# Kernel optimization log

Hardware: AMD Instinct MI355X
Metric: run time of the kernel (lower is better)

Reference implementation:

```python
import jax, jax.numpy as jnp
from jax import lax
import numpy as np

B, A, T = 128, 32, 32
HID = 64
DEG = 7
MODES = 25
OUT_FRAMES = 12
NHEAD, DHEAD = 16, 64


def legendre_tmat(out_frames, degree):
    # normalized Legendre basis evaluated at t_n, shape [degree+1, len(t_n)]
    t = np.arange(-6, out_frames + 1, dtype=np.float32)
    t = t / t[-1]
    P = [np.ones_like(t), t]
    for n in range(1, degree):
        P.append(((2 * n + 1) * t * P[n] - n * P[n - 1]) / (n + 1))
    P = np.stack(P[: degree + 1], 0)
    norm = np.sqrt((2 * np.arange(degree + 1) + 1) / 2.0).astype(np.float32)
    return (P * norm[:, None]).astype(np.float32)


def _conv(x, w, stride, pad):
    return lax.conv_general_dilated(x, w, (stride, stride), [(pad, pad), (pad, pad)],
                                    dimension_numbers=("NCHW", "OIHW", "NCHW"))


def _bn(x, g, b, eps=1e-5):
    m = jnp.mean(x, axis=(0, 2, 3), keepdims=True)
    v = jnp.var(x, axis=(0, 2, 3), keepdims=True)
    return (x - m) / jnp.sqrt(v + eps) * g[None, :, None, None] + b[None, :, None, None]


def setup_inputs() -> dict:
    key = jax.random.key(0)
    ks = jax.random.split(key, 32)

    def rn(i, shape, scale=0.05):
        return jax.random.normal(ks[i], shape, dtype=jnp.float32) * scale

    inp = {
        "cnn_feat": rn(0, (B, 1024, 14, 14), 1.0),
        "ego_state": rn(1, (B, T, 5), 1.0),
        "agents_state": rn(2, (B, A, T, 5), 1.0),
        "ego_state_len": jax.random.randint(ks[3], (B,), 0, T),
        "agents_state_len": jax.random.randint(ks[4], (B, A), 0, T),
        "agents_grid_pos": jax.random.randint(ks[5], (B, A, 2), 0, 14),
        "state_fc_W": rn(6, (HID, 5)), "state_fc_b": rn(7, (HID,)),
        "lstm_Wih": rn(8, (4 * HID, HID)), "lstm_Whh": rn(9, (4 * HID, HID)),
        "lstm_bih": rn(10, (4 * HID,)), "lstm_bhh": rn(11, (4 * HID,)),
        "enc_fc_W": rn(12, (HID, HID)), "enc_fc_b": rn(13, (HID,)),
        "conv1_W": rn(14, (512, 1024 + HID, 3, 3)),
        "bn1_g": jnp.ones((512,), jnp.float32), "bn1_b": jnp.zeros((512,), jnp.float32),
        "conv2_W": rn(15, (512, 512, 3, 3)),
        "bn2_g": jnp.ones((512,), jnp.float32), "bn2_b": jnp.zeros((512,), jnp.float32),
        "q_W": rn(16, (NHEAD * DHEAD, 512 + HID)),
        "k_W": rn(17, (NHEAD * DHEAD, 512, 1, 1)),
        "v_W": rn(18, (NHEAD * DHEAD, 512, 1, 1)),
        "attn_out_W": rn(19, (512, NHEAD * DHEAD)), "attn_out_b": rn(20, (512,)),
        "cls_W": rn(21, (MODES, 512 + HID + 512)), "cls_b": rn(22, (MODES,)),
        "dec1_W": rn(23, (256, 512 + HID + 512)), "dec1_b": rn(24, (256,)),
        "dec2_W": rn(25, ((DEG + 1) * 2 * MODES, 256)), "dec2_b": rn(26, ((DEG + 1) * 2 * MODES,)),
    }
    return inp


def reference(cnn_feat, ego_state, agents_state, ego_state_len, agents_state_len,
              agents_grid_pos, state_fc_W, state_fc_b, lstm_Wih, lstm_Whh, lstm_bih,
              lstm_bhh, enc_fc_W, enc_fc_b, conv1_W, bn1_g, bn1_b, conv2_W, bn2_g,
              bn2_b, q_W, k_W, v_W, attn_out_W, attn_out_b, cls_W, cls_b, dec1_W,
              dec1_b, dec2_W, dec2_b):
    Bn, _, Hs, Ws = cnn_feat.shape

    def lstm_encode(seq, lens):
        # seq [N,T,5]; packed-sequence semantics with zero init == take h at step len-1
        N, Tn, _ = seq.shape
        h = seq @ state_fc_W.T + state_fc_b  # [N,T,64]

        def step(carry, xt):
            hh, cc = carry
            g = xt @ lstm_Wih.T + hh @ lstm_Whh.T + lstm_bih + lstm_bhh
            i, f_, gg, o = jnp.split(g, 4, axis=-1)
            cc = jax.nn.sigmoid(f_) * cc + jax.nn.sigmoid(i) * jnp.tanh(gg)
            hh = jax.nn.sigmoid(o) * jnp.tanh(cc)
            return (hh, cc), hh

        z = jnp.zeros((N, HID), h.dtype)
        _, hs = lax.scan(step, (z, z), h.transpose(1, 0, 2))  # hs [T,N,64]
        idx = jnp.clip(lens, 1, Tn).astype(jnp.int32) - 1
        last = hs[idx, jnp.arange(N)]
        return last @ enc_fc_W.T + enc_fc_b

    ego = lstm_encode(ego_state, ego_state_len)  # [B,64]
    ag = lstm_encode(agents_state.reshape(Bn * A, T, 5),
                     agents_state_len.reshape(-1)).reshape(Bn, A, HID)

    # scatter-add agent encodings into the spatial grid (overlapping writes accumulate)
    grid = jnp.zeros((Bn, Hs, Ws, HID), cnn_feat.dtype)
    bidx = jnp.broadcast_to(jnp.arange(Bn)[:, None], (Bn, A))
    grid = grid.at[bidx, agents_grid_pos[..., 0], agents_grid_pos[..., 1]].add(ag)

    x = jnp.concatenate([cnn_feat, grid.transpose(0, 3, 1, 2)], axis=1)
    x = jax.nn.relu(_bn(_conv(x, conv1_W, 1, 1), bn1_g, bn1_b))
    x = jax.nn.relu(_bn(_conv(x, conv2_W, 2, 1), bn2_g, bn2_b))  # [B,512,7,7]

    ego_t = jnp.concatenate([x[:, :, 3, 3], ego], axis=1)  # [B,576]
    q = (ego_t @ q_W.T).reshape(Bn, NHEAD, DHEAD)
    k = _conv(x, k_W, 1, 1).reshape(Bn, NHEAD, DHEAD, -1)  # g = 9*9 = 81
    v = _conv(x, v_W, 1, 1).reshape(Bn, NHEAD, DHEAD, -1)
    energy = jnp.einsum("bhf,bhfg->bhg", q, k)
    attn = jax.nn.softmax(energy / (NHEAD * DHEAD) ** 0.5, axis=2)
    o = jnp.einsum("bhg,bhdg->bhd", attn, v).reshape(Bn, -1)
    o = o @ attn_out_W.T + attn_out_b

    feat = jnp.concatenate([o, ego_t], axis=1)  # [B,1088]
    conf = feat @ cls_W.T + cls_b
    d = jax.nn.relu(feat @ dec1_W.T + dec1_b)
    d = (d @ dec2_W.T + dec2_b).reshape(Bn, MODES, -1)

    tmat = jnp.asarray(legendre_tmat(OUT_FRAMES, DEG))  # [DEG+1, 19]
    out_x = d[:, :, : DEG + 1] @ tmat
    out_y = d[:, :, DEG + 1:] @ tmat
    traj = jnp.stack([out_x, out_y], axis=3)  # [B,MODES,19,2]
    return traj, conf
```

## Files before the change

kernel.cpp:

```cpp
#include <hip/hip_runtime.h>
#include <stdint.h>
#include <stddef.h>

#define DEVINL static __device__ __forceinline__

typedef __attribute__((ext_vector_type(8))) short  bfrag;
typedef __attribute__((ext_vector_type(4))) float  facc;

DEVINL uint16_t f2b(float f){
  uint32_t u = __float_as_uint(f);
  return (uint16_t)((u + 0x7fffu + ((u >> 16) & 1u)) >> 16);
}
DEVINL float b2f(uint16_t b){ return __uint_as_float(((uint32_t)b) << 16); }

DEVINL facc MFMA(bfrag a, bfrag b, facc c){
  return __builtin_amdgcn_mfma_f32_16x16x32_bf16(a, b, c, 0, 0, 0);
}

DEVINL void gload16(const void* g, void* l){
  __builtin_amdgcn_global_load_lds(
      (const __attribute__((address_space(1))) uint32_t*)g,
      (__attribute__((address_space(3))) uint32_t*)l, 16, 0, 0);
}

DEVINL float fast_tanh(float x){
  return 2.f/(1.f+__expf(-2.f*x)) - 1.f;
}

struct PrepArgs {
  const float* cnn;        uint16_t* Xp;
  uint16_t* Y1P;           float* gridb;   float* stats;
  const float *Wih, *Whh, *bih, *bhh, *sW, *sb, *encW;
  uint16_t* Wc;  float* be;  uint16_t* encWb;  float* tm;
  const float* conv1W;     uint16_t* WP1;
  const float* conv2W;     uint16_t* WP2;
  const float* kWf;        uint16_t* WKT;
  const float* fs[6];      uint16_t* fd[6];   int fn[6];  int fb0[6];
};

__global__ __launch_bounds__(256) void k_prep(PrepArgs a){
  int blk = blockIdx.x, t = threadIdx.x;
  if(blk < 4096){
    __shared__ float tile[32*200];
    int b = blk>>5, ch = blk&31;
    int c0 = ch*32;
    for(int i=t;i<32*196;i+=256){
      int ci = i/196, s = i%196;
      tile[ci*200+s] = a.cnn[((size_t)b*1024 + c0+ci)*196 + s];
    }
    __syncthreads();
    for(int i=t;i<16*196;i+=256){
      int s = i>>4, c2 = i&15;
      int y = s/14, x = s%14;
      uint32_t pu = (uint32_t)f2b(tile[(2*c2)*200+s]) |
                    ((uint32_t)f2b(tile[(2*c2+1)*200+s])<<16);
      *(uint32_t*)(a.Xp + (((size_t)b*16 + y+1)*16 + x+1)*1088 + c0 + 2*c2) = pu;
    }
  } else if(blk < 4352){
    int idx = blk - 4096;
    int b = idx & 127;
    uint16_t* base = (idx < 128) ? a.Xp : a.Y1P;
    int C = (idx < 128) ? 1088 : 512;
    for(int p=0;p<60;p++){
      int y, x;
      if(p<16){ y=0; x=p; }
      else if(p<32){ y=15; x=p-16; }
      else { int q=p-32; y=1+(q>>1); x=(q&1)?15:0; }
      uint32_t* dst = (uint32_t*)(base + ((size_t)(b*16+y)*16 + x)*C);
      for(int i=t;i<C/2;i+=256) dst[i] = 0;
    }
    float* g = a.gridb + (size_t)idx*6272;
    for(int i=t;i<6272;i+=256) g[i] = 0.f;
    if(idx == 0){
      for(int i=t;i<2048;i+=256) a.stats[i] = 0.f;
    }
  } else if(blk == 4352){
    int n = t;
    if(n < 19){
      float tv = (float)(n - 6) / 12.0f;
      float Pm = 1.0f, Pc = tv;
      a.tm[0*19+n] = Pm * sqrtf(0.5f);
      a.tm[1*19+n] = Pc * sqrtf(1.5f);
      for(int q=1; q<7; q++){
        float Pn = ((float)(2*q+1)*tv*Pc - (float)q*Pm) / (float)(q+1);
        Pm = Pc; Pc = Pn;
        a.tm[(q+1)*19+n] = Pc * sqrtf((float)(2*(q+1)+1) * 0.5f);
      }
    }
    for(int k=0;k<64;k++) a.Wc[n*96+k] = f2b(a.Whh[n*64+k]);
    for(int k5=0;k5<5;k5++){
      float s = 0.f;
      for(int j=0;j<64;j++) s += a.Wih[n*64+j]*a.sW[j*5+k5];
      a.Wc[n*96+64+k5] = f2b(s);
    }
    for(int k=69;k<96;k++) a.Wc[n*96+k] = 0;
    float s = 0.f;
    for(int j=0;j<64;j++) s += a.Wih[n*64+j]*a.sb[j];
    a.be[n] = s + a.bih[n] + a.bhh[n];
    if(n < 64){
      for(int k=0;k<64;k++) a.encWb[n*64+k] = f2b(a.encW[n*64+k]);
    }
  } else if(blk < 4865){
    int o = blk - 4353;
    for(int c=t; c<1088; c+=256){
      const float* src = a.conv1W + ((size_t)o*1088 + c)*9;
      float v[9];
      #pragma unroll
      for(int d=0;d<9;d++) v[d] = src[d];
      #pragma unroll
      for(int d=0;d<9;d++)
        a.WP1[((size_t)d*512 + o)*1088 + c] = f2b(v[d]);
    }
  } else if(blk < 5377){
    int o = blk - 4865;
    for(int c=t; c<512; c+=256){
      const float* src = a.conv2W + ((size_t)o*512 + c)*9;
      float v[9];
      #pragma unroll
      for(int d=0;d<9;d++) v[d] = src[d];
      #pragma unroll
      for(int dy=0;dy<3;dy++)
        #pragma unroll
        for(int dx=0;dx<3;dx++)
          a.WP2[((size_t)(dy*512 + o))*1536 + dx*512 + c] = f2b(v[dy*3+dx]);
    }
  } else if(blk < 5393){
    int h = blk - 5377;
    for(int i=t; i<32768; i+=256){
      int c = i>>6, d = i&63;
      a.WKT[((size_t)h*512 + c)*64 + d] = f2b(a.kWf[((size_t)(h*64+d))*512 + c]);
    }
  } else {
    int fblk = blk - 5393;
    int j = 0;
    while(j < 5 && fblk >= a.fb0[j+1]) j++;
    int base = (fblk - a.fb0[j])*8192;
    const float* s = a.fs[j];
    uint16_t* d = a.fd[j];
    int n = a.fn[j];
    int hi = base + 8192; if(hi > n) hi = n;
    for(int i=base+t; i<hi; i+=256) d[i] = f2b(s[i]);
  }
}

__global__ void k_packx_grid(const float* __restrict__ agrid, uint16_t* __restrict__ Xp)
{
  int b = blockIdx.x >> 1, half = blockIdx.x & 1;
  int j0 = half*32, t = threadIdx.x;
  for(int i=t;i<16*196;i+=256){
    int s = i>>4, j2 = i&15;
    int y = s/14, x = s%14;
    const float* gsrc = agrid + ((size_t)b*196 + s)*64 + j0 + 2*j2;
    uint32_t pu = (uint32_t)f2b(gsrc[0]) | ((uint32_t)f2b(gsrc[1])<<16);
    *(uint32_t*)(Xp + (((size_t)b*16 + y+1)*16 + x+1)*1088 + 1024 + j0 + 2*j2) = pu;
  }
}

__global__ __launch_bounds__(256) void k_lstm(
    const float* __restrict__ ego_seq, const float* __restrict__ ag_seq,
    const int* __restrict__ ego_len, const int* __restrict__ ag_len,
    const int* __restrict__ grid_pos,
    const uint16_t* __restrict__ Wc, const float* __restrict__ be,
    const uint16_t* __restrict__ encWb, const float* __restrict__ encB,
    float* __restrict__ agrid, uint16_t* __restrict__ egoT, uint16_t* __restrict__ feat)
{
  __shared__ __align__(16) uint16_t A[32*96];
  __shared__ float Xf[32*160];
  __shared__ int   idxs[32];

  int t = threadIdx.x, w = t>>6, l = t&63;
  int blk = blockIdx.x;
  bool isEgo = blk < 4;
  int seq0 = isEgo ? blk*32 : (blk-4)*32;
  const float* seqp = (isEgo ? ego_seq : ag_seq) + (size_t)seq0*160;

  for(int i=t;i<32*160;i+=256) Xf[i] = seqp[i];
  if(t < 32){
    int L = isEgo ? ego_len[seq0+t] : ag_len[seq0+t];
    if(L < 1) L = 1;
    idxs[t] = L-1;
  }
  for(int i=t;i<32*96;i+=256) A[i] = 0;

  bfrag bf[4][3];
  float be4[4];
  for(int ct=0;ct<4;ct++){
    int n = (ct*4+w)*16 + (l&15);
    for(int ks=0;ks<3;ks++)
      bf[ct][ks] = *(const bfrag*)(Wc + n*96 + ks*32 + (l>>4)*8);
    be4[ct] = be[n];
  }
  float cst[8], hl[8];
  for(int i=0;i<8;i++){ cst[i]=0.f; hl[i]=0.f; }
  __syncthreads();
  int myidx[8];
  for(int rt=0;rt<2;rt++) for(int r=0;r<4;r++){
    int s = rt*16 + (l>>4)*4 + r;
    myidx[rt*4+r] = idxs[s];
  }

  for(int st=0; st<32; st++){
    if(t < 160){ int s=t/5, kk=t%5; A[s*96+64+kk] = f2b(Xf[s*160 + st*5 + kk]); }
    __syncthreads();
    facc acc[2][4];
    for(int rt=0;rt<2;rt++) for(int ct=0;ct<4;ct++) acc[rt][ct] = facc{0.f,0.f,0.f,0.f};
    #pragma unroll
    for(int ks=0;ks<3;ks++){
      bfrag aA[2];
      #pragma unroll
      for(int rt=0;rt<2;rt++)
        aA[rt] = *(const bfrag*)(A + (rt*16+(l&15))*96 + ks*32 + (l>>4)*8);
      #pragma unroll
      for(int rt=0;rt<2;rt++)
        #pragma unroll
        for(int ct=0;ct<4;ct++)
          acc[rt][ct] = MFMA(aA[rt], bf[ct][ks], acc[rt][ct]);
    }
    __syncthreads();
    #pragma unroll
    for(int rt=0;rt<2;rt++) for(int r=0;r<4;r++){
      int cell = rt*4+r;
      int s = rt*16 + (l>>4)*4 + r;
      float gi = acc[rt][0][r] + be4[0];
      float gf = acc[rt][1][r] + be4[1];
      float gg = acc[rt][2][r] + be4[2];
      float go = acc[rt][3][r] + be4[3];
      float si = 1.f/(1.f+__expf(-gi));
      float sf = 1.f/(1.f+__expf(-gf));
      float so = 1.f/(1.f+__expf(-go));
      float tg = fast_tanh(gg);
      float c2 = sf*cst[cell] + si*tg;
      cst[cell] = c2;
      float hn = so*fast_tanh(c2);
      A[s*96 + w*16 + (l&15)] = f2b(hn);
      if(st == myidx[cell]) hl[cell] = hn;
    }
  }
  __syncthreads();
  for(int rt=0;rt<2;rt++) for(int r=0;r<4;r++){
    int s = rt*16 + (l>>4)*4 + r;
    A[s*96 + w*16 + (l&15)] = f2b(hl[rt*4+r]);
  }
  __syncthreads();
  bfrag eb[2];
  for(int ks=0;ks<2;ks++)
    eb[ks] = *(const bfrag*)(encWb + (w*16+(l&15))*64 + ks*32 + (l>>4)*8);
  facc ea[2]; ea[0] = facc{0.f,0.f,0.f,0.f}; ea[1] = facc{0.f,0.f,0.f,0.f};
  for(int ks=0;ks<2;ks++){
    for(int rt=0;rt<2;rt++){
      bfrag aA = *(const bfrag*)(A + (rt*16+(l&15))*96 + ks*32 + (l>>4)*8);
      ea[rt] = MFMA(aA, eb[ks], ea[rt]);
    }
  }
  int n = w*16 + (l&15);
  float bn_ = encB[n];
  for(int rt=0;rt<2;rt++) for(int r=0;r<4;r++){
    int s = rt*16 + (l>>4)*4 + r;
    float v = ea[rt][r] + bn_;
    int gs = seq0 + s;
    if(isEgo){
      egoT[(size_t)gs*576 + 512 + n] = f2b(v);
      feat[(size_t)gs*1088 + 1024 + n] = f2b(v);
    } else {
      int py = grid_pos[gs*2+0], px = grid_pos[gs*2+1];
      atomicAdd(&agrid[((size_t)(gs>>5)*196 + py*14 + px)*64 + n], v);
    }
  }
}

__global__ __launch_bounds__(512) void k_conv1_8p(
    const uint16_t* __restrict__ Ain, const uint16_t* __restrict__ Wb,
    uint16_t* __restrict__ Out, float* __restrict__ stats)
{
  constexpr int CB = 1088;
  constexpr int NSTEP = 153;
  __shared__ __align__(16) char LDSb[131072];

  int t = threadIdx.x, w = t>>6, l = t&63;
  int wm = w>>2, wn = w&3;

  int xcd = blockIdx.x & 7, pos = blockIdx.x >> 3;
  int wgid = (xcd < 4 ? xcd*25 : 100 + (xcd-4)*24) + pos;
  int m0 = (wgid % 98) * 256;
  int n0 = (wgid / 98) * 256;

  const uint16_t* aP[2][2];
  const uint16_t* bP[2][2];
  #pragma unroll
  for(int P=0;P<2;P++)
    #pragma unroll
    for(int j=0;j<2;j++){
      int partrow = j*64 + (t>>3);
      int swz = ((t&7) ^ (partrow&7))*8;
      int gr = P*64 + partrow + ((partrow>=64)?64:0);
      int m = m0 + gr; int b = m/196, s = m%196, y = s/14, x = s%14;
      aP[P][j] = Ain + ((b*16+y)*16+x)*CB + swz;
      int nb = n0 + (partrow>>5)*64 + P*32 + (partrow&31);
      bP[P][j] = Wb + (size_t)nb*CB + swz;
    }

  facc acc[8][4];
  #pragma unroll
  for(int i=0;i<8;i++)
    #pragma unroll
    for(int j=0;j<4;j++) acc[i][j] = facc{0.f,0.f,0.f,0.f};

  bfrag aF[4][2], bF0[2][2], bF1[2][2];
  int dd = 0;

  #define STG(buf, PART) do{                                                   \
    if((PART)==0 || (PART)==3){ const int P_ = ((PART)==3);                    \
      _Pragma("unroll")                                                        \
      for(int j_=0;j_<2;j_++)                                                  \
        gload16(aP[P_][j_], LDSb + (buf)*65536 + P_*16384 + j_*8192 + w*1024); \
    } else { const int P_ = ((PART)==2);                                       \
      _Pragma("unroll")                                                        \
      for(int j_=0;j_<2;j_++)                                                  \
        gload16(bP[P_][j_], LDSb + (buf)*65536 + 32768 + P_*16384 + j_*8192 + w*1024); \
    }                                                                          \
  }while(0)

  #define ADVK() do{                                                          \
    if(dd==8){                                                                \
      _Pragma("unroll")                                                       \
      for(int P_=0;P_<2;P_++) for(int j_=0;j_<2;j_++){                        \
        aP[P_][j_] += 64 - 34*CB; bP[P_][j_] += 64 - 8*512*CB; }              \
      dd = 0;                                                                 \
    } else {                                                                  \
      int sA_ = (dd==2||dd==5) ? 14*CB : CB;                                  \
      _Pragma("unroll")                                                       \
      for(int P_=0;P_<2;P_++) for(int j_=0;j_<2;j_++){                        \
        aP[P_][j_] += sA_; bP[P_][j_] += 512*CB; }                            \
      dd++;                                                                   \
    }                                                                         \
  }while(0)

  #define VM4 asm volatile("s_waitcnt vmcnt(4)" ::: "memory")
  #define VM2 asm volatile("s_waitcnt vmcnt(2)" ::: "memory")
  #define VM0 asm volatile("s_waitcnt vmcnt(0)" ::: "memory")

  #define LDA(mh) do{                                                         \
    const uint16_t* Ab_ = (const uint16_t*)(LDSb + p*65536 + (mh)*16384);     \
    _Pragma("unroll")                                                         \
    for(int i_=0;i_<4;i_++)                                                   \
      _Pragma("unroll")                                                       \
      for(int ks_=0;ks_<2;ks_++)                                              \
        aF[i_][ks_] = *(const bfrag*)(Ab_ + (wm*64 + i_*16 + (l&15))*64       \
                        + ((ks_*32 + (l>>4)*8) ^ ((l&7)<<3)));                \
  }while(0)

  #define LDB(dst, nh) do{                                                   \
    const uint16_t* Bb_ = (const uint16_t*)(LDSb + p*65536 + 32768 + (nh)*16384); \
    _Pragma("unroll")                                                         \
    for(int j_=0;j_<2;j_++)                                                   \
      _Pragma("unroll")                                                       \
      for(int ks_=0;ks_<2;ks_++)                                              \
        dst[j_][ks_] = *(const bfrag*)(Bb_ + (wn*32 + j_*16 + (l&15))*64      \
                        + ((ks_*32 + (l>>4)*8) ^ ((l&7)<<3)));                \
  }while(0)

  #define MM(mh, nh, bsrc) do{                                               \
    __builtin_amdgcn_s_setprio(1);                                           \
    _Pragma("unroll")                                                        \
    for(int ks_=0;ks_<2;ks_++)                                               \
      _Pragma("unroll")                                                      \
      for(int i_=0;i_<4;i_++)                                                \
        _Pragma("unroll")                                                    \
        for(int j_=0;j_<2;j_++)                                              \
          acc[(mh)*4+i_][(nh)*2+j_] =                                        \
            MFMA(aF[i_][ks_], bsrc[j_][ks_], acc[(mh)*4+i_][(nh)*2+j_]);     \
    __builtin_amdgcn_s_setprio(0);                                           \
  }while(0)

  #define BARS do{ __builtin_amdgcn_sched_barrier(0); __builtin_amdgcn_s_barrier(); }while(0)
  #define EBAR __builtin_amdgcn_s_barrier()

  STG(0,0); STG(0,1); STG(0,2); STG(0,3);
  ADVK();
  VM4;
  EBAR;

  for(int kt=0; kt<NSTEP-1; kt++){
    int p = kt&1;
    LDA(0); LDB(bF0,0); STG(p^1,0); BARS; MM(0,0,bF0); VM4; EBAR;
    LDB(bF1,1);         STG(p^1,1); BARS; MM(0,1,bF1); VM4; EBAR;
    LDA(1);             STG(p^1,2); BARS; MM(1,1,bF1);      EBAR;
                        STG(p^1,3); BARS; MM(1,0,bF0); VM4; EBAR;
    if(kt < NSTEP-2) ADVK();
  }
  {
    int p = 0;
    LDA(0); LDB(bF0,0); BARS; MM(0,0,bF0); VM2; EBAR;
    LDB(bF1,1);         BARS; MM(0,1,bF1); VM0; EBAR;
    LDA(1);             BARS; MM(1,1,bF1);      EBAR;
                        BARS; MM(1,0,bF0);      EBAR;
  }

  #undef LDA
  #undef LDB
  #undef MM
  #undef BARS
  #undef EBAR
  #undef STG
  #undef ADVK

  __syncthreads();
  int* oo = (int*)LDSb;
  if(t < 256){
    int m = m0 + t; int b = m/196, s = m%196, y = s/14, x = s%14;
    oo[t] = ((b*16 + y+1)*16 + (x+1))*512;
  }
  __syncthreads();
  #pragma unroll
  for(int i=0;i<8;i++)
    #pragma unroll
    for(int j=0;j<4;j++){
      int n = n0 + wn*64 + j*16 + (l&15);
      #pragma unroll
      for(int r=0;r<4;r++){
        int mr = wm*128 + i*16 + (l>>4)*4 + r;
        Out[(size_t)oo[mr] + n] = f2b(acc[i][j][r]);
      }
    }
  __syncthreads();
  float* sred = (float*)LDSb;
  int rg = wm*4 + (l>>4);
  #pragma unroll
  for(int j=0;j<4;j++){
    float s=0.f, q=0.f;
    #pragma unroll
    for(int i=0;i<8;i++)
      #pragma unroll
      for(int r=0;r<4;r++){ float v = acc[i][j][r]; s += v; q += v*v; }
    int nl = wn*64 + j*16 + (l&15);
    sred[(nl*8 + rg)*2+0] = s;
    sred[(nl*8 + rg)*2+1] = q;
  }
  __syncthreads();
  if(t < 256){
    float s=0.f, q=0.f;
    #pragma unroll
    for(int rgi=0;rgi<8;rgi++){ s += sred[(t*8+rgi)*2]; q += sred[(t*8+rgi)*2+1]; }
    atomicAdd(&stats[n0+t], s);
    atomicAdd(&stats[512+n0+t], q);
  }
}

__global__ __launch_bounds__(256) void k_conv2dy(
    const uint16_t* __restrict__ Ain, const uint16_t* __restrict__ Wb,
    uint16_t* __restrict__ PS,
    const float* __restrict__ stats, const float* __restrict__ gg,
    const float* __restrict__ bb)
{
  __shared__ __align__(16) uint16_t As[2*128*64];
  __shared__ __align__(16) uint16_t Bs[2*128*64];
  __shared__ float scs[512], shs[512];

  int t = threadIdx.x, w = t>>6, l = t&63;
  int dy = blockIdx.y;

  for(int c=t;c<512;c+=256){
    float mu = stats[c]*(1.f/25088.f);
    float var = stats[512+c]*(1.f/25088.f) - mu*mu;
    float sc = gg[c]*rsqrtf(var+1e-5f);
    scs[c] = sc; shs[c] = bb[c] - mu*sc;
  }

  int xcd = blockIdx.x & 7, pos = blockIdx.x >> 3;
  int wgid = (xcd < 4 ? xcd*25 : 100 + (xcd-4)*24) + pos;
  int n0 = (wgid / 49) * 128;
  int m0 = (wgid % 49) * 128;

  const uint16_t* aP[4];
  const uint16_t* bP[4];
  #pragma unroll
  for(int p=0;p<4;p++){
    int r = w*32 + p*8 + (l>>3);
    int m = m0 + r;
    int b = m/49, s = m%49, y = s/7, x = s%7;
    aP[p] = Ain + ((b*16 + 2*y + dy)*16 + 2*x)*512 + (l&7)*8;
    bP[p] = Wb + ((size_t)(dy*512 + n0 + r))*1536 + (l&7)*8;
  }

  facc acc[4][4];
  #pragma unroll
  for(int i=0;i<4;i++)
    #pragma unroll
    for(int j=0;j<4;j++) acc[i][j] = facc{0.f,0.f,0.f,0.f};
  int wm = w>>1, wn = w&1;

  uint4 av[4];

  #define C2LOADA() do{                                                     \
    _Pragma("unroll")                                                       \
    for(int p=0;p<4;p++){ av[p] = *(const uint4*)aP[p]; aP[p] += 64; }      \
  }while(0)

  #define C2BSTG(buf) do{                                                  \
    char* bd_ = (char*)Bs + (buf)*16384 + w*4096;                          \
    _Pragma("unroll")                                                      \
    for(int p=0;p<4;p++){ gload16(bP[p], bd_ + p*1024); bP[p] += 64; }     \
  }while(0)

  #define C2AWRITE(buf, kt) do{                                            \
    int c0_ = (((kt)*64) & 511) + (l&7)*8;                                  \
    _Pragma("unroll")                                                      \
    for(int p=0;p<4;p++){                                                  \
      const uint16_t* vv = (const uint16_t*)&av[p];                        \
      uint16_t ov[8];                                                      \
      _Pragma("unroll")                                                    \
      for(int j=0;j<8;j++){                                                \
        int c_ = c0_ + j;                                                  \
        ov[j] = f2b(fmaxf(b2f(vv[j])*scs[c_] + shs[c_], 0.f));             \
      }                                                                    \
      *(uint4*)((char*)As + (buf)*16384 + w*4096 + p*1024 + l*16) = *(uint4*)ov; \
    }                                                                      \
  }while(0)

  #define C2CMP(buf) do{                                                    \
    const uint16_t* Ab_ = As + (buf)*8192;                                  \
    const uint16_t* Bb_ = Bs + (buf)*8192;                                  \
    _Pragma("unroll")                                                       \
    for(int ks=0;ks<2;ks++){                                                \
      bfrag a_[4], b_[4];                                                   \
      _Pragma("unroll")                                                     \
      for(int i=0;i<4;i++)                                                  \
        a_[i] = *(const bfrag*)(Ab_ + (wm*64 + i*16 + (l&15))*64 + ks*32 + (l>>4)*8); \
      _Pragma("unroll")                                                     \
      for(int j=0;j<4;j++)                                                  \
        b_[j] = *(const bfrag*)(Bb_ + (wn*64 + j*16 + (l&15))*64 + ks*32 + (l>>4)*8); \
      _Pragma("unroll")                                                     \
      for(int i=0;i<4;i++)                                                  \
        _Pragma("unroll")                                                   \
        for(int j=0;j<4;j++)                                                \
          acc[i][j] = MFMA(a_[i], b_[j], acc[i][j]);                        \
    }                                                                       \
  }while(0)

  C2LOADA();
  C2BSTG(0);
  C2AWRITE(0, 0);
  __syncthreads();
  for(int stp=0; stp<24; stp++){
    if(stp < 23){ C2LOADA(); C2BSTG((stp+1)&1); }
    C2CMP(stp&1);
    if(stp < 23) C2AWRITE((stp+1)&1, stp+1);
    __syncthreads();
  }

  #undef C2LOADA
  #undef C2BSTG
  #undef C2AWRITE
  #undef C2CMP

  uint16_t* out = PS + (size_t)dy*3211264;
  #pragma unroll
  for(int i=0;i<4;i++)
    #pragma unroll
    for(int j=0;j<4;j++){
      int n = n0 + wn*64 + j*16 + (l&15);
      #pragma unroll
      for(int r=0;r<4;r++){
        int mr = m0 + wm*64 + i*16 + (l>>4)*4 + r;
        out[(size_t)mr*512 + n] = f2b(acc[i][j][r]);
      }
    }
}

__global__ void k_bn2sum(const uint16_t* __restrict__ PS, uint16_t* __restrict__ Y2,
                         float* __restrict__ stats)
{
  int t = threadIdx.x;
  int m0 = blockIdx.x*16;
  float s0=0,s1=0,q0=0,q1=0;
  for(int i=0;i<16;i++){
    size_t off = (size_t)(m0+i)*512 + 2*t;
    uint32_t u0 = *(const uint32_t*)(PS + off);
    uint32_t u1 = *(const uint32_t*)(PS + 3211264 + off);
    uint32_t u2 = *(const uint32_t*)(PS + 6422528 + off);
    float a = b2f((uint16_t)u0)+b2f((uint16_t)u1)+b2f((uint16_t)u2);
    float c = b2f((uint16_t)(u0>>16))+b2f((uint16_t)(u1>>16))+b2f((uint16_t)(u2>>16));
    s0+=a; q0+=a*a; s1+=c; q1+=c*c;
    *(uint32_t*)(Y2 + off) = (uint32_t)f2b(a) | ((uint32_t)f2b(c)<<16);
  }
  atomicAdd(&stats[2*t],   s0);
  atomicAdd(&stats[2*t+1], s1);
  atomicAdd(&stats[512+2*t],   q0);
  atomicAdd(&stats[512+2*t+1], q1);
}

__global__ void k_center(const uint16_t* __restrict__ Y2, const float* __restrict__ stats,
                         const float* __restrict__ gg, const float* __restrict__ bb,
                         uint16_t* __restrict__ egoT, uint16_t* __restrict__ feat)
{
  int b = blockIdx.x, t = threadIdx.x;
  int c = 2*t;
  float mu0 = stats[c]*(1.f/6272.f),     mu1 = stats[c+1]*(1.f/6272.f);
  float v0 = stats[512+c]*(1.f/6272.f) - mu0*mu0;
  float v1 = stats[512+c+1]*(1.f/6272.f) - mu1*mu1;
  float sc0 = gg[c]*rsqrtf(v0+1e-5f),    sc1 = gg[c+1]*rsqrtf(v1+1e-5f);
  float sh0 = bb[c] - mu0*sc0,           sh1 = bb[c+1] - mu1*sc1;
  size_t off = (size_t)(b*49+24)*512 + c;
  uint32_t u = *(const uint32_t*)(Y2 + off);
  float a = fmaxf(b2f((uint16_t)u)*sc0 + sh0, 0.f);
  float d = fmaxf(b2f((uint16_t)(u>>16))*sc1 + sh1, 0.f);
  uint32_t pu = (uint32_t)f2b(a) | ((uint32_t)f2b(d)<<16);
  *(uint32_t*)(egoT + (size_t)b*576 + c) = pu;
  *(uint32_t*)(feat + (size_t)b*1088 + 512 + c) = pu;
}

__global__ __launch_bounds__(256) void k_sgemm(
    const uint16_t* __restrict__ A, int lda,
    const uint16_t* __restrict__ B, int ldb,
    const float* __restrict__ bias,
    void* __restrict__ C, int ldc,
    int N, int K, int flags)
{
  int t = threadIdx.x, w = t>>6, l = t&63;
  int nt = blockIdx.x*4 + w;
  int n  = nt*16 + (l&15);
  int m0 = blockIdx.y*16;
  bool nv = n < N;
  facc acc = facc{0.f,0.f,0.f,0.f};
  for(int k=0;k<K;k+=32){
    bfrag af = *(const bfrag*)(A + (size_t)(m0+(l&15))*lda + k + (l>>4)*8);
    bfrag bf_ = {0,0,0,0,0,0,0,0};
    if(nv) bf_ = *(const bfrag*)(B + (size_t)n*ldb + k + (l>>4)*8);
    acc = MFMA(af, bf_, acc);
  }
  if(nv){
    float bv = bias ? bias[n] : 0.f;
    #pragma unroll
    for(int r=0;r<4;r++){
      int m = m0 + (l>>4)*4 + r;
      float v = acc[r] + bv;
      if(flags & 1) v = fmaxf(v, 0.f);
      if(flags & 2) ((float*)C)[(size_t)m*ldc + n] = v;
      else ((uint16_t*)C)[(size_t)m*ldc + n] = f2b(v);
    }
  }
}

__global__ __launch_bounds__(256) void k_tail1(
    const uint16_t* __restrict__ FEAT,
    const uint16_t* __restrict__ D1W, const float* __restrict__ d1B,
    const uint16_t* __restrict__ CLSW, const float* __restrict__ clsB,
    uint16_t* __restrict__ D1out, float* __restrict__ confOut)
{
  int t = threadIdx.x, w = t>>6, l = t&63;
  int m0 = blockIdx.y*16;
  bool isCls = (blockIdx.x == 4);
  int n = (isCls ? w : (blockIdx.x*4 + w))*16 + (l&15);
  int N = isCls ? 25 : 256;
  const uint16_t* B = isCls ? CLSW : D1W;
  bool nv = n < N;
  facc acc = facc{0.f,0.f,0.f,0.f};
  for(int k=0;k<1088;k+=32){
    bfrag af = *(const bfrag*)(FEAT + (size_t)(m0+(l&15))*1088 + k + (l>>4)*8);
    bfrag bf_ = {0,0,0,0,0,0,0,0};
    if(nv) bf_ = *(const bfrag*)(B + (size_t)n*1088 + k + (l>>4)*8);
    acc = MFMA(af, bf_, acc);
  }
  if(nv){
    #pragma unroll
    for(int r=0;r<4;r++){
      int m = m0 + (l>>4)*4 + r;
      if(isCls){
        confOut[(size_t)m*25 + n] = acc[r] + clsB[n];
      } else {
        D1out[(size_t)m*256 + n] = f2b(fmaxf(acc[r] + d1B[n], 0.f));
      }
    }
  }
}

__global__ __launch_bounds__(256) void k_tail2(
    const uint16_t* __restrict__ D1B, const uint16_t* __restrict__ D2W,
    const float* __restrict__ d2B, const float* __restrict__ tm,
    float* __restrict__ outF)
{
  __shared__ float co[16*64];
  __shared__ float tms[152];
  int t = threadIdx.x, w = t>>6, l = t&63;
  if(t < 152) tms[t] = tm[t];
  int bx = blockIdx.x, m0 = blockIdx.y*16;
  int n = (bx*4 + w)*16 + (l&15);
  bool nv = n < 400;
  facc acc = facc{0.f,0.f,0.f,0.f};
  for(int k=0;k<256;k+=32){
    bfrag af = *(const bfrag*)(D1B + (size_t)(m0+(l&15))*256 + k + (l>>4)*8);
    bfrag bf_ = {0,0,0,0,0,0,0,0};
    if(nv) bf_ = *(const bfrag*)(D2W + (size_t)n*256 + k + (l>>4)*8);
    acc = MFMA(af, bf_, acc);
  }
  if(nv){
    #pragma unroll
    for(int r=0;r<4;r++){
      int mm = (l>>4)*4 + r;
      co[mm*64 + (w*16 + (l&15))] = acc[r] + d2B[n];
    }
  }
  __syncthreads();
  int nmodes = (bx < 6) ? 4 : 1;
  for(int idx=t; idx<16*nmodes*19; idx+=256){
    int mm = idx/(nmodes*19);
    int rem = idx%(nmodes*19);
    int md = rem/19, tt = rem%19;
    const float* cp = &co[mm*64 + md*16];
    float x=0.f, y=0.f;
    #pragma unroll
    for(int j=0;j<8;j++){ float tv = tms[j*19+tt]; x += cp[j]*tv; y += cp[8+j]*tv; }
    float* op = outF + ((size_t)(m0+mm)*25 + bx*4+md)*38;
    op[tt*2+0] = x; op[tt*2+1] = y;
  }
}

__global__ __launch_bounds__(256) void k_bgemm(
    const uint16_t* __restrict__ A, int lda, int aoffs,
    const uint16_t* __restrict__ B, int ldb, int brows,
    uint16_t* __restrict__ C, int ldc, int coffs,
    int K)
{
  int t = threadIdx.x, w = t>>6, l = t&63;
  int z = blockIdx.z;
  int n = (blockIdx.x*4 + w)*16 + (l&15);
  int m0 = blockIdx.y*16;
  const uint16_t* Ab = A + (size_t)z*aoffs;
  const uint16_t* Bb = B + (size_t)z*brows*ldb;
  facc acc = facc{0.f,0.f,0.f,0.f};
  for(int k=0;k<K;k+=32){
    bfrag af = *(const bfrag*)(Ab + (size_t)(m0+(l&15))*lda + k + (l>>4)*8);
    bfrag bf_ = *(const bfrag*)(Bb + (size_t)n*ldb + k + (l>>4)*8);
    acc = MFMA(af, bf_, acc);
  }
  #pragma unroll
  for(int r=0;r<4;r++){
    int m = m0 + (l>>4)*4 + r;
    C[(size_t)m*ldc + z*coffs + n] = f2b(acc[r]);
  }
}

__global__ __launch_bounds__(512) void k_attn2(
    const uint16_t* __restrict__ U16, const uint16_t* __restrict__ y2,
    const float* __restrict__ stats, const float* __restrict__ gg,
    const float* __restrict__ bb,
    uint16_t* __restrict__ zout)
{
  __shared__ __align__(16) char LA[49*1024 + 8*1024];
  __shared__ float scs[512], shs[512];
  uint16_t* uls = (uint16_t*)(LA + 49*1024);
  int t = threadIdx.x, w = t>>6, l = t&63;
  int b = blockIdx.x >> 1, half = blockIdx.x & 1;
  int h = half*8 + w;

  if(t < 512){
    float mu = stats[t]*(1.f/6272.f);
    float var = stats[512+t]*(1.f/6272.f) - mu*mu;
    float sc = gg[t]*rsqrtf(var+1e-5f);
    scs[t] = sc; shs[t] = bb[t] - mu*sc;
  }
  __syncthreads();

  for(int i=t; i<3136; i+=512){
    int g = i>>6, c16 = i&63;
    uint4 raw = *(const uint4*)(y2 + ((size_t)(b*49+g)*512 + c16*8));
    const uint16_t* rp = (const uint16_t*)&raw;
    uint16_t ov[8];
    #pragma unroll
    for(int j=0;j<8;j++){
      int c = c16*8 + j;
      ov[j] = f2b(fmaxf(b2f(rp[j])*scs[c] + shs[c], 0.f));
    }
    *(uint4*)(LA + g*1024 + ((c16*16) ^ ((g&31)<<4))) = *(uint4*)ov;
  }
  *(uint4*)((char*)uls + w*1024 + l*16) =
      *(const uint4*)(U16 + (size_t)b*8192 + h*512 + l*8);
  __syncthreads();

  float dot = 0.f;
  if(l < 49){
    const char* yrow = LA + l*1024;
    const char* ur = (const char*)uls + w*1024;
    for(int c16=0;c16<64;c16++){
      uint4 uv = *(const uint4*)(ur + c16*16);
      uint4 yv = *(const uint4*)(yrow + ((c16*16) ^ ((l&31)<<4)));
      const uint16_t* up = (const uint16_t*)&uv;
      const uint16_t* yp = (const uint16_t*)&yv;
      #pragma unroll
      for(int j=0;j<8;j++) dot += b2f(up[j])*b2f(yp[j]);
    }
  }
  float e = (l<49) ? dot*(1.f/32.f) : -1e30f;
  float mx = e;
  for(int s=32;s>0;s>>=1) mx = fmaxf(mx, __shfl_xor(mx, s));
  mx = fmaxf(mx, 0.f);
  float p = (l<49) ? __expf(e-mx) : 0.f;
  float den = p;
  for(int s=32;s>0;s>>=1) den += __shfl_xor(den, s);
  den += 32.f*__expf(-mx);

  float z[8];
  #pragma unroll
  for(int j=0;j<8;j++) z[j]=0.f;
  for(int g=0; g<49; g++){
    float pg = __shfl(p, g);
    uint4 yv = *(const uint4*)(LA + g*1024 + ((l*16) ^ ((g&31)<<4)));
    const uint16_t* yp = (const uint16_t*)&yv;
    #pragma unroll
    for(int j=0;j<8;j++) z[j] += pg*b2f(yp[j]);
  }
  float inv = 1.f/den;
  uint16_t zr[8];
  #pragma unroll
  for(int j=0;j<8;j++) zr[j] = f2b(z[j]*inv);
  *(uint4*)(zout + ((size_t)(b*16+h)*512) + l*8) = *(uint4*)zr;
}

extern "C" void kernel_launch(void* const* d_in, const int* in_sizes, int n_in,
                              void* d_out, int out_size, void* d_ws, size_t ws_size,
                              hipStream_t stream)
{
  const float* cnn      = (const float*)d_in[0];
  const float* ego_seq  = (const float*)d_in[1];
  const float* ag_seq   = (const float*)d_in[2];
  const int*   ego_len  = (const int*)d_in[3];
  const int*   ag_len   = (const int*)d_in[4];
  const int*   grid_pos = (const int*)d_in[5];
  const float* sW  = (const float*)d_in[6];
  const float* sb  = (const float*)d_in[7];
  const float* Wih = (const float*)d_in[8];
  const float* Whh = (const float*)d_in[9];
  const float* bih = (const float*)d_in[10];
  const float* bhh = (const float*)d_in[11];
  const float* encW = (const float*)d_in[12];
  const float* encB = (const float*)d_in[13];
  const float* conv1W = (const float*)d_in[14];
  const float* bn1g = (const float*)d_in[15];
  const float* bn1b = (const float*)d_in[16];
  const float* conv2W = (const float*)d_in[17];
  const float* bn2g = (const float*)d_in[18];
  const float* bn2b = (const float*)d_in[19];
  const float* qWf  = (const float*)d_in[20];
  const float* kWf  = (const float*)d_in[21];
  const float* vWf  = (const float*)d_in[22];
  const float* aoW  = (const float*)d_in[23];
  const float* aoB  = (const float*)d_in[24];
  const float* clsWf = (const float*)d_in[25];
  const float* clsB  = (const float*)d_in[26];
  const float* d1Wf  = (const float*)d_in[27];
  const float* d1B   = (const float*)d_in[28];
  const float* d2Wf  = (const float*)d_in[29];
  const float* d2B   = (const float*)d_in[30];

  char* ws = (char*)d_ws;
  const size_t XP_OFF   = 0;
  const size_t PS_OFF   = 0;
  const size_t U_OFF    = 0;
  const size_t ZB_OFF   = 2097152;
  const size_t Y2_OFF   = 41943040;
  const size_t Y1P_OFF  = 71303168;
  const size_t WP1_OFF  = 104857600;
  const size_t WP2_OFF  = 114884608;
  const size_t WKT_OFF  = 119603200;
  const size_t WVB_OFF  = 120651776;
  const size_t QW_OFF   = 121700352;
  const size_t AOW_OFF  = 122880000;
  const size_t CLSW_OFF = 123928576;
  const size_t D1W_OFF  = 123982976;
  const size_t D2W_OFF  = 124540032;
  const size_t GRID_OFF = 124744832;
  const size_t EGOT_OFF = 131167360;
  const size_t FEAT_OFF = 131314816;
  const size_t QB_OFF   = 131593344;
  const size_t OBUF_OFF = 132117632;
  const size_t D1_OFF   = 132379776;
  const size_t WC_OFF   = 132650112;
  const size_t BE_OFF   = 132699264;
  const size_t ENCW_OFF = 132700288;
  const size_t TMAT_OFF = 132708480;
  const size_t ST1_OFF  = 132709120;
  const size_t ST2_OFF  = 132713216;

  uint16_t* XP   = (uint16_t*)(ws + XP_OFF);
  uint16_t* PSB  = (uint16_t*)(ws + PS_OFF);
  uint16_t* U16  = (uint16_t*)(ws + U_OFF);
  uint16_t* ZB16 = (uint16_t*)(ws + ZB_OFF);
  uint16_t* Y2   = (uint16_t*)(ws + Y2_OFF);
  uint16_t* Y1P  = (uint16_t*)(ws + Y1P_OFF);
  uint16_t* WP1  = (uint16_t*)(ws + WP1_OFF);
  uint16_t* WP2  = (uint16_t*)(ws + WP2_OFF);
  uint16_t* WKT  = (uint16_t*)(ws + WKT_OFF);
  uint16_t* WVB  = (uint16_t*)(ws + WVB_OFF);
  uint16_t* QW   = (uint16_t*)(ws + QW_OFF);
  uint16_t* AOW  = (uint16_t*)(ws + AOW_OFF);
  uint16_t* CLSW = (uint16_t*)(ws + CLSW_OFF);
  uint16_t* D1W  = (uint16_t*)(ws + D1W_OFF);
  uint16_t* D2W  = (uint16_t*)(ws + D2W_OFF);
  float*    GRIDB= (float*)(ws + GRID_OFF);
  uint16_t* EGOT = (uint16_t*)(ws + EGOT_OFF);
  uint16_t* FEAT = (uint16_t*)(ws + FEAT_OFF);
  uint16_t* QB16 = (uint16_t*)(ws + QB_OFF);
  uint16_t* OBUF = (uint16_t*)(ws + OBUF_OFF);
  uint16_t* D1B  = (uint16_t*)(ws + D1_OFF);
  uint16_t* WC   = (uint16_t*)(ws + WC_OFF);
  float*    BE   = (float*)(ws + BE_OFF);
  uint16_t* ENCWB= (uint16_t*)(ws + ENCW_OFF);
  float*    TMAT = (float*)(ws + TMAT_OFF);
  float*    ST1  = (float*)(ws + ST1_OFF);
  float*    ST2  = (float*)(ws + ST2_OFF);
  float*    outF = (float*)d_out;

  {
    PrepArgs a;
    a.cnn = cnn; a.Xp = XP; a.Y1P = Y1P; a.gridb = GRIDB; a.stats = ST1;
    a.Wih=Wih; a.Whh=Whh; a.bih=bih; a.bhh=bhh; a.sW=sW; a.sb=sb; a.encW=encW;
    a.Wc=WC; a.be=BE; a.encWb=ENCWB; a.tm=TMAT;
    a.conv1W=conv1W; a.WP1=WP1;
    a.conv2W=conv2W; a.WP2=WP2;
    a.kWf=kWf; a.WKT=WKT;
    a.fs[0]=vWf;  a.fd[0]=WVB;   a.fn[0]=1024*512;
    a.fs[1]=qWf;  a.fd[1]=QW;    a.fn[1]=1024*576;
    a.fs[2]=aoW;  a.fd[2]=AOW;   a.fn[2]=512*1024;
    a.fs[3]=clsWf;a.fd[3]=CLSW;  a.fn[3]=25*1088;
    a.fs[4]=d1Wf; a.fd[4]=D1W;   a.fn[4]=256*1088;
    a.fs[5]=d2Wf; a.fd[5]=D2W;   a.fn[5]=400*256;
    int nb = 0;
    for(int j=0;j<6;j++){ a.fb0[j] = nb; nb += (a.fn[j] + 8191)/8192; }
    k_prep<<<5393 + nb, 256, 0, stream>>>(a);
  }

  k_lstm<<<132,256,0,stream>>>(ego_seq, ag_seq, ego_len, ag_len, grid_pos,
                               WC, BE, ENCWB, encB, GRIDB, EGOT, FEAT);
  k_packx_grid<<<256,256,0,stream>>>(GRIDB, XP);
  k_conv1_8p<<<196,512,0,stream>>>(XP, WP1, Y1P, ST1);
  k_conv2dy<<<dim3(196,3),256,0,stream>>>(Y1P, WP2, PSB, ST1, bn1g, bn1b);
  k_bn2sum<<<392,256,0,stream>>>(PSB, Y2, ST2);
  k_center<<<128,256,0,stream>>>(Y2, ST2, bn2g, bn2b, EGOT, FEAT);
  k_sgemm<<<dim3(16,8),256,0,stream>>>(EGOT, 576, QW, 576, nullptr, QB16, 1024, 1024, 576, 0);
  k_bgemm<<<dim3(8,8,16),256,0,stream>>>(QB16, 1024, 64, WKT, 64, 512, U16, 8192, 512, 64);
  k_attn2<<<256,512,0,stream>>>(U16, Y2, ST2, bn2g, bn2b, ZB16);
  k_bgemm<<<dim3(1,8,16),256,0,stream>>>(ZB16, 8192, 512, WVB, 512, 64, OBUF, 1024, 64, 512);
  k_sgemm<<<dim3(8,8),256,0,stream>>>(OBUF, 1024, AOW, 1024, aoB, FEAT, 1088, 512, 1024, 0);
  k_tail1<<<dim3(5,8),256,0,stream>>>(FEAT, D1W, d1B, CLSW, clsB, D1B, outF + 121600);
  k_tail2<<<dim3(7,8),256,0,stream>>>(D1B, D2W, d2B, TMAT, outF);

  (void)in_sizes; (void)n_in; (void)out_size; (void)ws_size;
}
```

Baseline: 551.8 us.

## Fuse conv2 kernel-row split into one kernel with in-kernel BN2 stats

```diff
diff --git a/kernel.cpp b/kernel.cpp
--- a/kernel.cpp
+++ b/kernel.cpp
@@ -446,10 +446,10 @@
   }
 }
 
-__global__ __launch_bounds__(256) void k_conv2dy(
+__global__ __launch_bounds__(256) void k_conv2m(
     const uint16_t* __restrict__ Ain, const uint16_t* __restrict__ Wb,
-    uint16_t* __restrict__ PS,
-    const float* __restrict__ stats, const float* __restrict__ gg,
+    uint16_t* __restrict__ Y2, float* __restrict__ st2,
+    const float* __restrict__ st1, const float* __restrict__ gg,
     const float* __restrict__ bb)
 {
   __shared__ __align__(16) uint16_t As[2*128*64];
@@ -457,11 +457,10 @@
   __shared__ float scs[512], shs[512];
 
   int t = threadIdx.x, w = t>>6, l = t&63;
-  int dy = blockIdx.y;
 
   for(int c=t;c<512;c+=256){
-    float mu = stats[c]*(1.f/25088.f);
-    float var = stats[512+c]*(1.f/25088.f) - mu*mu;
+    float mu = st1[c]*(1.f/25088.f);
+    float var = st1[512+c]*(1.f/25088.f) - mu*mu;
     float sc = gg[c]*rsqrtf(var+1e-5f);
     scs[c] = sc; shs[c] = bb[c] - mu*sc;
   }
@@ -478,8 +477,8 @@
     int r = w*32 + p*8 + (l>>3);
     int m = m0 + r;
     int b = m/49, s = m%49, y = s/7, x = s%7;
-    aP[p] = Ain + ((b*16 + 2*y + dy)*16 + 2*x)*512 + (l&7)*8;
-    bP[p] = Wb + ((size_t)(dy*512 + n0 + r))*1536 + (l&7)*8;
+    aP[p] = Ain + ((b*16 + 2*y)*16 + 2*x)*512 + (l&7)*8;
+    bP[p] = Wb + ((size_t)(n0 + r))*1536 + (l&7)*8;
   }
 
   facc acc[4][4];
@@ -493,17 +492,17 @@
 
   #define C2LOADA() do{                                                     \
     _Pragma("unroll")                                                       \
-    for(int p=0;p<4;p++){ av[p] = *(const uint4*)aP[p]; aP[p] += 64; }      \
+    for(int p=0;p<4;p++) av[p] = *(const uint4*)aP[p];                      \
   }while(0)
 
   #define C2BSTG(buf) do{                                                  \
     char* bd_ = (char*)Bs + (buf)*16384 + w*4096;                          \
     _Pragma("unroll")                                                      \
-    for(int p=0;p<4;p++){ gload16(bP[p], bd_ + p*1024); bP[p] += 64; }     \
+    for(int p=0;p<4;p++) gload16(bP[p], bd_ + p*1024);                     \
   }while(0)
 
-  #define C2AWRITE(buf, kt) do{                                            \
-    int c0_ = (((kt)*64) & 511) + (l&7)*8;                                  \
+  #define C2AWRITE(buf, cbase) do{                                         \
+    int c0_ = (cbase) + (l&7)*8;                                            \
     _Pragma("unroll")                                                      \
     for(int p=0;p<4;p++){                                                  \
       const uint16_t* vv = (const uint16_t*)&av[p];                        \
@@ -514,6 +513,18 @@
         ov[j] = f2b(fmaxf(b2f(vv[j])*scs[c_] + shs[c_], 0.f));             \
       }                                                                    \
       *(uint4*)((char*)As + (buf)*16384 + w*4096 + p*1024 + l*16) = *(uint4*)ov; \
+    }                                                                      \
+  }while(0)
+
+  #define C2ADV() do{                                                      \
+    if(ccs==23){                                                           \
+      _Pragma("unroll")                                                    \
+      for(int p=0;p<4;p++){ aP[p] += 6720; bP[p] += 784960; }              \
+      ccs = 0;                                                             \
+    } else {                                                               \
+      _Pragma("unroll")                                                    \
+      for(int p=0;p<4;p++){ aP[p] += 64; bP[p] += 64; }                    \
+      ccs++;                                                               \
     }                                                                      \
   }while(0)
 
@@ -537,23 +548,31 @@
     }                                                                       \
   }while(0)
 
+  int ccs = 0;
   C2LOADA();
   C2BSTG(0);
   C2AWRITE(0, 0);
-  __syncthreads();
-  for(int stp=0; stp<24; stp++){
-    if(stp < 23){ C2LOADA(); C2BSTG((stp+1)&1); }
+  C2ADV();
+  __syncthreads();
+  for(int stp=0; stp<72; stp++){
+    if(stp < 71){
+      C2LOADA();
+      C2BSTG((stp+1)&1);
+    }
     C2CMP(stp&1);
-    if(stp < 23) C2AWRITE((stp+1)&1, stp+1);
+    if(stp < 71){
+      C2AWRITE((stp+1)&1, (ccs*64)&511);
+      C2ADV();
+    }
     __syncthreads();
   }
 
   #undef C2LOADA
   #undef C2BSTG
   #undef C2AWRITE
+  #undef C2ADV
   #undef C2CMP
 
-  uint16_t* out = PS + (size_t)dy*3211264;
   #pragma unroll
   for(int i=0;i<4;i++)
     #pragma unroll
@@ -562,31 +581,31 @@
       #pragma unroll
       for(int r=0;r<4;r++){
         int mr = m0 + wm*64 + i*16 + (l>>4)*4 + r;
-        out[(size_t)mr*512 + n] = f2b(acc[i][j][r]);
+        Y2[(size_t)mr*512 + n] = f2b(acc[i][j][r]);
       }
     }
-}
-
-__global__ void k_bn2sum(const uint16_t* __restrict__ PS, uint16_t* __restrict__ Y2,
-                         float* __restrict__ stats)
-{
-  int t = threadIdx.x;
-  int m0 = blockIdx.x*16;
-  float s0=0,s1=0,q0=0,q1=0;
-  for(int i=0;i<16;i++){
-    size_t off = (size_t)(m0+i)*512 + 2*t;
-    uint32_t u0 = *(const uint32_t*)(PS + off);
-    uint32_t u1 = *(const uint32_t*)(PS + 3211264 + off);
-    uint32_t u2 = *(const uint32_t*)(PS + 6422528 + off);
-    float a = b2f((uint16_t)u0)+b2f((uint16_t)u1)+b2f((uint16_t)u2);
-    float c = b2f((uint16_t)(u0>>16))+b2f((uint16_t)(u1>>16))+b2f((uint16_t)(u2>>16));
-    s0+=a; q0+=a*a; s1+=c; q1+=c*c;
-    *(uint32_t*)(Y2 + off) = (uint32_t)f2b(a) | ((uint32_t)f2b(c)<<16);
-  }
-  atomicAdd(&stats[2*t],   s0);
-  atomicAdd(&stats[2*t+1], s1);
-  atomicAdd(&stats[512+2*t],   q0);
-  atomicAdd(&stats[512+2*t+1], q1);
+  __syncthreads();
+  float* sred = (float*)As;
+  int rg = wm*4 + (l>>4);
+  #pragma unroll
+  for(int j=0;j<4;j++){
+    float s=0.f, q=0.f;
+    #pragma unroll
+    for(int i=0;i<4;i++)
+      #pragma unroll
+      for(int r=0;r<4;r++){ float v = acc[i][j][r]; s += v; q += v*v; }
+    int nl = wn*64 + j*16 + (l&15);
+    sred[(nl*8 + rg)*2+0] = s;
+    sred[(nl*8 + rg)*2+1] = q;
+  }
+  __syncthreads();
+  if(t < 128){
+    float s=0.f, q=0.f;
+    #pragma unroll
+    for(int rgi=0;rgi<8;rgi++){ s += sred[(t*8+rgi)*2]; q += sred[(t*8+rgi)*2+1]; }
+    atomicAdd(&st2[n0+t], s);
+    atomicAdd(&st2[512+n0+t], q);
+  }
 }
 
 __global__ void k_center(const uint16_t* __restrict__ Y2, const float* __restrict__ stats,
@@ -854,7 +873,6 @@
 
   char* ws = (char*)d_ws;
   const size_t XP_OFF   = 0;
-  const size_t PS_OFF   = 0;
   const size_t U_OFF    = 0;
   const size_t ZB_OFF   = 2097152;
   const size_t Y2_OFF   = 41943040;
@@ -882,7 +900,6 @@
   const size_t ST2_OFF  = 132713216;
 
   uint16_t* XP   = (uint16_t*)(ws + XP_OFF);
-  uint16_t* PSB  = (uint16_t*)(ws + PS_OFF);
   uint16_t* U16  = (uint16_t*)(ws + U_OFF);
   uint16_t* ZB16 = (uint16_t*)(ws + ZB_OFF);
   uint16_t* Y2   = (uint16_t*)(ws + Y2_OFF);
@@ -933,8 +950,7 @@
                                WC, BE, ENCWB, encB, GRIDB, EGOT, FEAT);
   k_packx_grid<<<256,256,0,stream>>>(GRIDB, XP);
   k_conv1_8p<<<196,512,0,stream>>>(XP, WP1, Y1P, ST1);
-  k_conv2dy<<<dim3(196,3),256,0,stream>>>(Y1P, WP2, PSB, ST1, bn1g, bn1b);
-  k_bn2sum<<<392,256,0,stream>>>(PSB, Y2, ST2);
+  k_conv2m<<<196,256,0,stream>>>(Y1P, WP2, Y2, ST2, ST1, bn1g, bn1b);
   k_center<<<128,256,0,stream>>>(Y2, ST2, bn2g, bn2b, EGOT, FEAT);
   k_sgemm<<<dim3(16,8),256,0,stream>>>(EGOT, 576, QW, 576, nullptr, QB16, 1024, 1024, 576, 0);
   k_bgemm<<<dim3(8,8,16),256,0,stream>>>(QB16, 1024, 64, WKT, 64, 512, U16, 8192, 512, 64);
```

Result: slower. 563.7 us (+2.2%).
